# Kernel tuning notes

Hardware: AMD Instinct MI355X
Metric: run time of the kernel (lower is better)

The kernel has to match this reference:

```python
import jax, jax.numpy as jnp
import numpy as np

N_NODES = 50000
N_EDGES = 800000
IN_CH = 64
HID = 128
OUT_CH = 1
NUM_LAYERS = 3
NUM_TIMESTEPS = 3
EDGE_DIM = 25
NUM_GRAPHS = 1024
NEG = 0.01  # leaky_relu negative slope (torch default & GATConv arg)


def leaky(v):
    return jnp.where(v >= 0, v, NEG * v)


def seg_softmax(a, idx, n):
    # PyG softmax: exp(a - max_per_segment) / (sum_per_segment + 1e-16)
    m = jax.ops.segment_max(a, idx, num_segments=n)
    m = jnp.where(jnp.isfinite(m), m, 0.0)  # guard empty segments
    e = jnp.exp(a - m[idx])
    s = jax.ops.segment_sum(e, idx, num_segments=n)
    return e / (s[idx] + 1e-16)


def gru(inp, h, Wih, Whh, bih, bhh):
    gi = inp @ Wih.T + bih
    gh = h @ Whh.T + bhh
    ir, iz, inn = jnp.split(gi, 3, axis=-1)
    hr, hz, hn = jnp.split(gh, 3, axis=-1)
    r = jax.nn.sigmoid(ir + hr)
    z = jax.nn.sigmoid(iz + hz)
    n = jnp.tanh(inn + r * hn)
    return (1.0 - z) * n + z * h


def setup_inputs() -> dict:
    key = jax.random.key(0)
    ks = iter(jax.random.split(key, 40))

    def nrm(shape, s=0.05):
        return jax.random.normal(next(ks), shape, dtype=jnp.float32) * s

    L = NUM_LAYERS - 1
    H3 = 3 * HID
    inp = dict(
        x=jax.random.normal(next(ks), (N_NODES, IN_CH), dtype=jnp.float32),
        edge_index=jax.random.randint(next(ks), (2, N_EDGES), 0, N_NODES),
        batch=jnp.sort(jax.random.randint(next(ks), (N_NODES,), 0, NUM_GRAPHS)),
        W1=nrm((HID, IN_CH)), b1=jnp.zeros((HID,), jnp.float32),
        Wg1=nrm((HID, HID + EDGE_DIM)), att_l=nrm((HID,)), att_r=nrm((HID,)),
        Wg2=nrm((HID, HID)), bg=jnp.zeros((HID,), jnp.float32),
        Wih0=nrm((H3, HID)), Whh0=nrm((H3, HID)),
        bih0=jnp.zeros((H3,), jnp.float32), bhh0=jnp.zeros((H3,), jnp.float32),
        Wa=nrm((L, HID, HID)), att_src_a=nrm((L, HID)), att_dst_a=nrm((L, HID)),
        ba=jnp.zeros((L, HID), jnp.float32),
        Wih_a=nrm((L, H3, HID)), Whh_a=nrm((L, H3, HID)),
        bih_a=jnp.zeros((L, H3), jnp.float32), bhh_a=jnp.zeros((L, H3), jnp.float32),
        Wm=nrm((HID, HID)), att_src_m=nrm((HID,)), att_dst_m=nrm((HID,)),
        bm=jnp.zeros((HID,), jnp.float32),
        Wih_m=nrm((H3, HID)), Whh_m=nrm((H3, HID)),
        bih_m=jnp.zeros((H3,), jnp.float32), bhh_m=jnp.zeros((H3,), jnp.float32),
        W2=nrm((OUT_CH, HID)), b2=jnp.zeros((OUT_CH,), jnp.float32),
    )
    return inp


def reference(x, edge_index, batch, W1, b1, Wg1, att_l, att_r, Wg2, bg,
              Wih0, Whh0, bih0, bhh0, Wa, att_src_a, att_dst_a, ba,
              Wih_a, Whh_a, bih_a, bhh_a, Wm, att_src_m, att_dst_m, bm,
              Wih_m, Whh_m, bih_m, bhh_m, W2, b2):
    N = x.shape[0]
    E = edge_index.shape[1]
    src, dst = edge_index[0], edge_index[1]  # j -> i, aggregate at i=dst
    edge_attr = jnp.ones((E, EDGE_DIM), dtype=x.dtype)  # built inside original forward

    x = leaky(x @ W1.T + b1)

    # GATEConv: edge-feature-aware attention, sum aggregation
    xe = leaky(jnp.concatenate([x[src], edge_attr], axis=-1) @ Wg1.T)  # [E, H]
    a = seg_softmax(leaky(xe @ att_l + (x @ att_r)[dst]), dst, N)
    msg = (x[src] @ Wg2.T) * a[:, None]
    h = jax.nn.elu(jax.ops.segment_sum(msg, dst, num_segments=N) + bg)
    x = jax.nn.relu(gru(h, x, Wih0, Whh0, bih0, bhh0))

    # (num_layers - 1) GATConv + GRU atom updates
    for l in range(NUM_LAYERS - 1):
        xt = x @ Wa[l].T
        a = seg_softmax(leaky((xt @ att_src_a[l])[src] + (xt @ att_dst_a[l])[dst]), dst, N)
        h = jax.nn.elu(jax.ops.segment_sum(xt[src] * a[:, None], dst, num_segments=N) + ba[l])
        x = jax.nn.relu(gru(h, x, Wih_a[l], Whh_a[l], bih_a[l], bhh_a[l]))

    # attentive readout: bipartite GATConv node->molecule over num_timesteps
    out = jax.nn.relu(jax.ops.segment_sum(x, batch, num_segments=NUM_GRAPHS))
    xt = x @ Wm.T                 # shared lin for src (fixed across timesteps)
    a_src = xt @ att_src_m        # [N]
    for _ in range(NUM_TIMESTEPS):
        ot = out @ Wm.T           # shared lin for dst
        a = seg_softmax(leaky(a_src + (ot @ att_dst_m)[batch]), batch, NUM_GRAPHS)
        h = jax.nn.elu(jax.ops.segment_sum(xt * a[:, None], batch, num_segments=NUM_GRAPHS) + bm)
        out = jax.nn.relu(gru(h, out, Wih_m, Whh_m, bih_m, bhh_m))

    return out @ W2.T + b2
```

## Files before the change

kernel.cpp:

```cpp
#include <hip/hip_runtime.h>
#include <math.h>

#define NN 50000
#define NE 800000
#define NG 1024
#define HID 128

typedef __attribute__((ext_vector_type(8))) short short8;
typedef __attribute__((ext_vector_type(4))) unsigned short ushort4v;
typedef __attribute__((ext_vector_type(4))) float f32x4;

__device__ __forceinline__ float leakyf(float v){ return v >= 0.f ? v : 0.01f*v; }
__device__ __forceinline__ float sigmf(float v){ return 1.f/(1.f+expf(-v)); }
__device__ __forceinline__ float eluf(float v){ return v > 0.f ? v : expm1f(v); }
__device__ __forceinline__ unsigned short bf16rne(float f){
  union { float f; unsigned u; } v; v.f = f;
  return (unsigned short)((v.u + 0x7FFFu + ((v.u >> 16) & 1u)) >> 16);
}
__device__ __forceinline__ float bf2f(unsigned short h){
  union { unsigned u; float f; } v; v.u = ((unsigned)h) << 16; return v.f;
}
__device__ __forceinline__ short8 cvt8(const float* a){
  short8 r;
#pragma unroll
  for (int j=0;j<8;j++) r[j] = (short)bf16rne(a[j]);
  return r;
}

__global__ __launch_bounds__(256)
void pack_all(const float* W1, const float* Wg1, const float* Wg2, const float* Wa,
              const float* Wm, const float* Wih0, const float* Whh0,
              const float* Wih_a, const float* Whh_a, const float* Wih_m,
              const float* Whh_m, unsigned short* __restrict__ dst)
{
  int m = (int)blockIdx.y;
  int t = (int)blockIdx.x*4 + ((int)threadIdx.x>>6);
  int l = (int)threadIdx.x & 63;
  const float* src; int stride=128, M=128, K=128; size_t doff;
  switch(m){
    case 0:  src=W1;    stride=64;  K=64;  doff=0;      break;
    case 1:  src=Wg1;   stride=153;        doff=8192;   break;
    case 2:  src=Wg2;                      doff=24576;  break;
    case 3:  src=Wa;                       doff=40960;  break;
    case 4:  src=Wa+16384;                 doff=57344;  break;
    case 5:  src=Wm;                       doff=73728;  break;
    case 6:  src=Wih0;  M=384;             doff=90112;  break;
    case 7:  src=Whh0;  M=384;             doff=139264; break;
    case 8:  src=Wih_a; M=384;             doff=188416; break;
    case 9:  src=Whh_a; M=384;             doff=237568; break;
    case 10: src=Wih_a+49152; M=384;       doff=286720; break;
    case 11: src=Whh_a+49152; M=384;       doff=335872; break;
    case 12: src=Wih_m; M=384;             doff=385024; break;
    default: src=Whh_m; M=384;             doff=434176; break;
  }
  int tk = K/32;
  if (t >= (M/16)*tk) return;
  int ct = t / tk, kc = t % tk;
  int row = ct*16 + (l&15);
  int col = kc*32 + ((l>>4)<<3);
  unsigned short o[8];
#pragma unroll
  for (int j=0;j<8;j++) o[j] = bf16rne(src[(size_t)row*stride + col + j]);
  ushort4v* d = (ushort4v*)(dst + doff + (((size_t)t*64 + l)<<3));
  ushort4v d0; d0.x=o[0]; d0.y=o[1]; d0.z=o[2]; d0.w=o[3];
  ushort4v d1; d1.x=o[4]; d1.y=o[5]; d1.z=o[6]; d1.w=o[7];
  d[0]=d0; d[1]=d1;
}

__global__ __launch_bounds__(256)
void gemm_f32(const float* __restrict__ A, const unsigned short* __restrict__ Wp,
              const float* __restrict__ bias, float* __restrict__ Cf,
              unsigned short* __restrict__ Cb, int rows, int act)
{
  constexpr int K = 64, KC = 2;
  const int tid=(int)threadIdx.x, w=tid>>6, l=tid&63;
  const int fr=l&15, fq=l>>4;
  const int rt=w>>1, ch=w&1;
  const int bn = (int)blockIdx.x*32;
  const int ar = bn + rt*16 + fr;
  f32x4 acc[4];
#pragma unroll
  for (int j=0;j<4;j++) acc[j] = (f32x4){0.f,0.f,0.f,0.f};
#pragma unroll
  for (int kc=0;kc<KC;kc++){
    float a8[8];
    if (ar < rows){
      *(float4*)&a8[0] = *(const float4*)(A + (size_t)ar*K + kc*32 + fq*8);
      *(float4*)&a8[4] = *(const float4*)(A + (size_t)ar*K + kc*32 + fq*8 + 4);
    } else {
#pragma unroll
      for (int j=0;j<8;j++) a8[j]=0.f;
    }
    short8 fa = cvt8(a8);
#pragma unroll
    for (int j=0;j<4;j++){
      const short8 bfr = *(const short8*)(Wp + ((((size_t)(ch*4+j)*KC + kc)*64 + l)<<3));
      acc[j] = __builtin_amdgcn_mfma_f32_16x16x32_bf16(fa, bfr, acc[j], 0, 0, 0);
    }
  }
#pragma unroll
  for (int j=0;j<4;j++){
    int c = ch*64 + j*16 + fr;
    float bv = bias ? bias[c] : 0.f;
#pragma unroll
    for (int r4=0;r4<4;r4++){
      float o = acc[j][r4] + bv;
      if (act) o = leakyf(o);
      int r = bn + rt*16 + fq*4 + r4;
      if (r < rows){
        Cf[(size_t)r*HID + c] = o;
        Cb[(size_t)r*HID + c] = bf16rne(o);
      }
    }
  }
}

__global__ __launch_bounds__(256)
void gemm_b16(const unsigned short* __restrict__ Ab, const unsigned short* __restrict__ Wp,
              const float* __restrict__ bias, unsigned short* __restrict__ Cb,
              const float* __restrict__ v1, const float* __restrict__ v2,
              const float* __restrict__ va,
              float* __restrict__ s1, float* __restrict__ s2, int rows, int act)
{
  __shared__ float sd1[2][32];
  __shared__ float sd2[2][32];
  constexpr int KC = 4;
  const int tid=(int)threadIdx.x, w=tid>>6, l=tid&63;
  const int fr=l&15, fq=l>>4;
  const int rt=w>>1, ch=w&1;
  const int bn = (int)blockIdx.x*32;
  const int ar = bn + rt*16 + fr;
  f32x4 acc[4];
#pragma unroll
  for (int j=0;j<4;j++) acc[j] = (f32x4){0.f,0.f,0.f,0.f};
  float pa = 0.f;
#pragma unroll
  for (int kc=0;kc<KC;kc++){
    short8 fa;
    if (ar < rows) fa = *(const short8*)(Ab + (size_t)ar*HID + kc*32 + fq*8);
    else { short8 z = {0,0,0,0,0,0,0,0}; fa = z; }
    if (va && ch==0){
      float4 t0 = *(const float4*)(va + kc*32 + fq*8);
      float4 t1 = *(const float4*)(va + kc*32 + fq*8 + 4);
      pa += bf2f((unsigned short)fa[0])*t0.x + bf2f((unsigned short)fa[1])*t0.y
          + bf2f((unsigned short)fa[2])*t0.z + bf2f((unsigned short)fa[3])*t0.w
          + bf2f((unsigned short)fa[4])*t1.x + bf2f((unsigned short)fa[5])*t1.y
          + bf2f((unsigned short)fa[6])*t1.z + bf2f((unsigned short)fa[7])*t1.w;
    }
#pragma unroll
    for (int j=0;j<4;j++){
      const short8 bfr = *(const short8*)(Wp + ((((size_t)(ch*4+j)*KC + kc)*64 + l)<<3));
      acc[j] = __builtin_amdgcn_mfma_f32_16x16x32_bf16(fa, bfr, acc[j], 0, 0, 0);
    }
  }
  float dp1[4]={0.f,0.f,0.f,0.f}, dp2[4]={0.f,0.f,0.f,0.f};
#pragma unroll
  for (int j=0;j<4;j++){
    int c = ch*64 + j*16 + fr;
    float bv = bias ? bias[c] : 0.f;
    float w1 = v1 ? v1[c] : 0.f;
    float w2 = v2 ? v2[c] : 0.f;
#pragma unroll
    for (int r4=0;r4<4;r4++){
      float o = acc[j][r4] + bv;
      if (act) o = leakyf(o);
      dp1[r4] += o*w1; dp2[r4] += o*w2;
      int r = bn + rt*16 + fq*4 + r4;
      if (r < rows && Cb) Cb[(size_t)r*HID + c] = bf16rne(o);
    }
  }
  if (v1){
#pragma unroll
    for (int r4=0;r4<4;r4++){
#pragma unroll
      for (int m=1;m<16;m<<=1){ dp1[r4] += __shfl_xor(dp1[r4], m); dp2[r4] += __shfl_xor(dp2[r4], m); }
    }
    if (fr==0){
#pragma unroll
      for (int r4=0;r4<4;r4++){
        sd1[ch][rt*16 + fq*4 + r4] = dp1[r4];
        sd2[ch][rt*16 + fq*4 + r4] = dp2[r4];
      }
    }
    __syncthreads();
    if (tid < 32){
      int r = bn + tid;
      if (r < rows) s1[r] = sd1[0][tid] + sd1[1][tid];
    } else if (v2 && tid < 64){
      int r = bn + tid - 32;
      if (r < rows) s2[r] = sd2[0][tid-32] + sd2[1][tid-32];
    }
  }
  if (va && ch==0){
    pa += __shfl_xor(pa, 16); pa += __shfl_xor(pa, 32);
    if (fq==0){
      int r = bn + rt*16 + fr;
      if (r < rows) s2[r] = pa;
    }
  }
}

__global__ __launch_bounds__(512, 2)
void fused_gru(const unsigned short* __restrict__ Ahb, const unsigned short* __restrict__ Axb,
               const float* __restrict__ Axf,
               const unsigned short* __restrict__ Wi, const unsigned short* __restrict__ Wh,
               const float* __restrict__ bih, const float* __restrict__ bhh,
               float* __restrict__ outf, unsigned short* __restrict__ outb, int tiles)
{
  const int tid=(int)threadIdx.x, w=tid>>6, l=tid&63;
  const int fr=l&15, fq=l>>4;
  short8 wi_r[3][4], wh_r[3][4];
#pragma unroll
  for (int g=0;g<3;g++)
#pragma unroll
    for (int kc=0;kc<4;kc++){
      size_t o = ((((size_t)(g*8 + w)*4 + kc)*64 + l)<<3);
      wi_r[g][kc] = *(const short8*)(Wi + o);
      wh_r[g][kc] = *(const short8*)(Wh + o);
    }
  const int c0 = w*16 + fr;
  float bi0=bih[c0], bi1=bih[c0+128], bi2=bih[c0+256];
  float bh0=bhh[c0], bh1=bhh[c0+128], bh2=bhh[c0+256];

  int rt_end = min((int)blockIdx.x*8 + 8, tiles);
  for (int rt = (int)blockIdx.x*8; rt < rt_end; rt++){
    const int bn = rt*16;
    const int arow = bn + fr;
    f32x4 ai0={0,0,0,0}, ai1={0,0,0,0}, ai2={0,0,0,0};
    f32x4 ah0={0,0,0,0}, ah1={0,0,0,0}, ah2={0,0,0,0};
#pragma unroll
    for (int kc=0;kc<4;kc++){
      short8 fa = *(const short8*)(Ahb + (size_t)arow*HID + kc*32 + fq*8);
      short8 fx = *(const short8*)(Axb + (size_t)arow*HID + kc*32 + fq*8);
      ai0 = __builtin_amdgcn_mfma_f32_16x16x32_bf16(fa, wi_r[0][kc], ai0, 0, 0, 0);
      ai1 = __builtin_amdgcn_mfma_f32_16x16x32_bf16(fa, wi_r[1][kc], ai1, 0, 0, 0);
      ai2 = __builtin_amdgcn_mfma_f32_16x16x32_bf16(fa, wi_r[2][kc], ai2, 0, 0, 0);
      ah0 = __builtin_amdgcn_mfma_f32_16x16x32_bf16(fx, wh_r[0][kc], ah0, 0, 0, 0);
      ah1 = __builtin_amdgcn_mfma_f32_16x16x32_bf16(fx, wh_r[1][kc], ah1, 0, 0, 0);
      ah2 = __builtin_amdgcn_mfma_f32_16x16x32_bf16(fx, wh_r[2][kc], ah2, 0, 0, 0);
    }
#pragma unroll
    for (int r4=0;r4<4;r4++){
      int row = bn + fq*4 + r4;
      float rr = sigmf(ai0[r4] + bi0 + ah0[r4] + bh0);
      float zz = sigmf(ai1[r4] + bi1 + ah1[r4] + bh1);
      float nn = tanhf(ai2[r4] + bi2 + rr*(ah2[r4] + bh2));
      float hv = Axf[(size_t)row*HID + c0];
      float o = fmaxf((1.f - zz)*nn + zz*hv, 0.f);
      outf[(size_t)row*HID + c0] = o;
      outb[(size_t)row*HID + c0] = bf16rne(o);
    }
  }
}

__global__ __launch_bounds__(256)
void rowdot(const float* __restrict__ A, const float* __restrict__ v,
            const float* __restrict__ bias, float* __restrict__ out, int rows)
{
  int wave = (int)((blockIdx.x * blockDim.x + threadIdx.x) >> 6);
  int lane = (int)(threadIdx.x & 63);
  if (wave >= rows) return;
  float2 a  = ((const float2*)(A + (size_t)wave*HID))[lane];
  float2 vv = ((const float2*)v)[lane];
  float s = a.x*vv.x + a.y*vv.y;
  for (int off=32; off; off>>=1) s += __shfl_down(s, off);
  if (lane==0) out[wave] = s + (bias ? bias[0] : 0.f);
}

__global__ void colvec(const float* __restrict__ W, const float* __restrict__ v,
                       float* __restrict__ out)
{
  int k = (int)threadIdx.x;
  float s = 0.f;
  for (int j=0;j<HID;j++) s += W[j*HID+k]*v[j];
  out[k] = s;
}

__global__ void prep_cg(const float* __restrict__ Wg1, float* __restrict__ cg){
  int j = (int)threadIdx.x;
  float s = 0.f;
  for (int k=128;k<153;k++) s += Wg1[j*153+k];
  cg[j] = s;
}

__global__ void count_kernel(const int* __restrict__ idx, int* __restrict__ cnt, int n){
  int i = (int)(blockIdx.x*blockDim.x + threadIdx.x);
  if (i < n) atomicAdd(&cnt[idx[i]], 1);
}

__global__ __launch_bounds__(1024)
void scan_blocks(const int* __restrict__ cnt, int* __restrict__ off,
                 int* __restrict__ tot, int n)
{
  __shared__ int buf[1024];
  int i = (int)(blockIdx.x*1024 + threadIdx.x);
  int v = (i<n)? cnt[i] : 0;
  buf[threadIdx.x] = v;
  __syncthreads();
  for (int s=1;s<1024;s<<=1){
    int t = ((int)threadIdx.x >= s) ? buf[threadIdx.x - s] : 0;
    __syncthreads();
    buf[threadIdx.x] += t;
    __syncthreads();
  }
  if (i<n) off[i] = buf[threadIdx.x] - v;
  if (threadIdx.x==1023) tot[blockIdx.x] = buf[1023];
}

__global__ void scan_tot(int* __restrict__ tot, int* __restrict__ off_end, int nb){
  int lane = (int)threadIdx.x;
  int orig = (lane<nb)? tot[lane] : 0;
  int v = orig;
  for (int s=1;s<64;s<<=1){ int t = __shfl_up(v, s); if (lane>=s) v += t; }
  int total = __shfl(v, 63);
  if (lane<nb) tot[lane] = v - orig;
  if (lane==0) *off_end = total;
}

__global__ void scan_add(int* __restrict__ off, const int* __restrict__ tot, int n){
  int i = (int)(blockIdx.x*blockDim.x + threadIdx.x);
  if (i<n) off[i] += tot[i>>10];
}

__global__ void fill_kernel(const int* __restrict__ src, const int* __restrict__ dst,
                            const int* __restrict__ off, int* __restrict__ fill,
                            int* __restrict__ ssrc, int n){
  int e = (int)(blockIdx.x*blockDim.x + threadIdx.x);
  if (e < n){
    int d = dst[e];
    int p = off[d] + atomicAdd(&fill[d], 1);
    ssrc[p] = src[e];
  }
}

__global__ void graph_bounds(const int* __restrict__ batch, int* __restrict__ goff){
  int g = (int)(blockIdx.x*blockDim.x + threadIdx.x);
  if (g > NG) return;
  int lo=0, hi=NN;
  while (lo<hi){ int mid=(lo+hi)>>1; if (batch[mid] < g) lo=mid+1; else hi=mid; }
  goff[g] = lo;
}

__global__ __launch_bounds__(256)
void agg_edges(const int* __restrict__ off, const int* __restrict__ ssrc,
               const float* __restrict__ ls, const float* __restrict__ ld,
               const unsigned short* __restrict__ Mrows, const float* __restrict__ bias,
               unsigned short* __restrict__ outb, int n)
{
  __shared__ float wbuf[4][64];
  __shared__ int   sbuf[4][64];
  const int ws = (int)(threadIdx.x >> 6);
  int node = (int)((blockIdx.x * blockDim.x + threadIdx.x) >> 6);
  int lane = (int)(threadIdx.x & 63);
  if (node >= n) return;
  int e0 = off[node], e1 = off[node+1];
  float ldv = ld[node];
  const int h = lane >> 5, cl = lane & 31;
  float denom = 0.f;
  float4 acc = make_float4(0.f,0.f,0.f,0.f);
  for (int j0=e0; j0<e1; j0+=64){
    int cnt = min(64, e1-j0);
    float wv = 0.f; int sc = 0;
    if (lane < cnt){
      sc = ssrc[j0+lane];
      wv = expf(leakyf(ls[sc]+ldv));
    }
    denom += wv;
    wbuf[ws][lane] = wv;
    sbuf[ws][lane] = sc;
#pragma unroll 4
    for (int k2=0;k2<cnt;k2+=2){
      float wk = wbuf[ws][k2+h];
      int  sck = sbuf[ws][k2+h];
      uint2 mm = *(const uint2*)(Mrows + (size_t)sck*HID + cl*4);
      acc.x += wk*bf2f((unsigned short)(mm.x&0xffff));
      acc.y += wk*bf2f((unsigned short)(mm.x>>16));
      acc.z += wk*bf2f((unsigned short)(mm.y&0xffff));
      acc.w += wk*bf2f((unsigned short)(mm.y>>16));
    }
  }
  acc.x += __shfl_xor(acc.x, 32); acc.y += __shfl_xor(acc.y, 32);
  acc.z += __shfl_xor(acc.z, 32); acc.w += __shfl_xor(acc.w, 32);
  for (int o=32;o;o>>=1) denom += __shfl_xor(denom, o);
  if (h==0){
    float inv = 1.f/(denom + 1e-16f);
    float4 b = *(const float4*)(bias + cl*4);
    ushort4v ob;
    ob.x = bf16rne(eluf(acc.x*inv + b.x));
    ob.y = bf16rne(eluf(acc.y*inv + b.y));
    ob.z = bf16rne(eluf(acc.z*inv + b.z));
    ob.w = bf16rne(eluf(acc.w*inv + b.w));
    *(ushort4v*)(outb + (size_t)node*HID + cl*4) = ob;
  }
}

__global__ __launch_bounds__(256)
void graph_sum(const int* __restrict__ goff, const float* __restrict__ X,
               float* __restrict__ outf, unsigned short* __restrict__ outb)
{
  int g = (int)((blockIdx.x*blockDim.x + threadIdx.x) >> 6);
  int lane = (int)(threadIdx.x & 63);
  if (g >= NG) return;
  float2 acc = make_float2(0.f,0.f);
  for (int n=goff[g]; n<goff[g+1]; ++n){
    float2 v = ((const float2*)(X + (size_t)n*HID))[lane];
    acc.x += v.x; acc.y += v.y;
  }
  float ox = fmaxf(acc.x,0.f), oy = fmaxf(acc.y,0.f);
  ((float2*)(outf + (size_t)g*HID))[lane] = make_float2(ox, oy);
  unsigned u = (unsigned)bf16rne(ox) | ((unsigned)bf16rne(oy) << 16);
  *(unsigned*)(outb + (size_t)g*HID + lane*2) = u;
}

__global__ __launch_bounds__(256)
void graph_soft2(const int* __restrict__ goff, const float* __restrict__ asrc,
                 const float* __restrict__ gout, const float* __restrict__ vmd,
                 const unsigned short* __restrict__ Xt, const float* __restrict__ bias,
                 unsigned short* __restrict__ outb)
{
  __shared__ float wbuf[4][64];
  const int ws = (int)(threadIdx.x >> 6);
  int g = (int)((blockIdx.x*blockDim.x + threadIdx.x) >> 6);
  int lane = (int)(threadIdx.x & 63);
  if (g >= NG) return;
  float2 ov = ((const float2*)(gout + (size_t)g*HID))[lane];
  float2 vv = ((const float2*)vmd)[lane];
  float ad = ov.x*vv.x + ov.y*vv.y;
  for (int o=32;o;o>>=1) ad += __shfl_xor(ad, o);
  int n0 = goff[g], n1 = goff[g+1];
  const int h = lane >> 5, cl = lane & 31;
  float denom = 0.f;
  float4 acc = make_float4(0.f,0.f,0.f,0.f);
  for (int j0=n0; j0<n1; j0+=64){
    int cnt = min(64, n1-j0);
    float wv = 0.f;
    if (lane < cnt) wv = expf(leakyf(asrc[j0+lane]+ad));
    denom += wv;
    wbuf[ws][lane] = wv;
#pragma unroll 4
    for (int k2=0;k2<cnt;k2+=2){
      float wk = wbuf[ws][k2+h];
      int rowi = min(j0 + k2 + h, n1 - 1);
      uint2 mm = *(const uint2*)(Xt + (size_t)rowi*HID + cl*4);
      acc.x += wk*bf2f((unsigned short)(mm.x&0xffff));
      acc.y += wk*bf2f((unsigned short)(mm.x>>16));
      acc.z += wk*bf2f((unsigned short)(mm.y&0xffff));
      acc.w += wk*bf2f((unsigned short)(mm.y>>16));
    }
  }
  acc.x += __shfl_xor(acc.x, 32); acc.y += __shfl_xor(acc.y, 32);
  acc.z += __shfl_xor(acc.z, 32); acc.w += __shfl_xor(acc.w, 32);
  for (int o=32;o;o>>=1) denom += __shfl_xor(denom, o);
  if (h==0){
    float inv = 1.f/(denom + 1e-16f);
    float4 b = *(const float4*)(bias + cl*4);
    ushort4v ob;
    ob.x = bf16rne(eluf(acc.x*inv + b.x));
    ob.y = bf16rne(eluf(acc.y*inv + b.y));
    ob.z = bf16rne(eluf(acc.z*inv + b.z));
    ob.w = bf16rne(eluf(acc.w*inv + b.w));
    *(ushort4v*)(outb + (size_t)g*HID + cl*4) = ob;
  }
}

extern "C" void kernel_launch(void* const* d_in, const int* in_sizes, int n_in,
                              void* d_out, int out_size, void* d_ws, size_t ws_size,
                              hipStream_t stream)
{
  const float* x_in  = (const float*)d_in[0];
  const int*   ei    = (const int*)d_in[1];
  const int*   batch = (const int*)d_in[2];
  const float* W1    = (const float*)d_in[3];
  const float* b1    = (const float*)d_in[4];
  const float* Wg1   = (const float*)d_in[5];
  const float* att_l = (const float*)d_in[6];
  const float* att_r = (const float*)d_in[7];
  const float* Wg2   = (const float*)d_in[8];
  const float* bg    = (const float*)d_in[9];
  const float* Wih0  = (const float*)d_in[10];
  const float* Whh0  = (const float*)d_in[11];
  const float* bih0  = (const float*)d_in[12];
  const float* bhh0  = (const float*)d_in[13];
  const float* Wa    = (const float*)d_in[14];
  const float* att_src_a = (const float*)d_in[15];
  const float* att_dst_a = (const float*)d_in[16];
  const float* ba    = (const float*)d_in[17];
  const float* Wih_a = (const float*)d_in[18];
  const float* Whh_a = (const float*)d_in[19];
  const float* bih_a = (const float*)d_in[20];
  const float* bhh_a = (const float*)d_in[21];
  const float* Wm    = (const float*)d_in[22];
  const float* att_src_m = (const float*)d_in[23];
  const float* att_dst_m = (const float*)d_in[24];
  const float* bm    = (const float*)d_in[25];
  const float* Wih_m = (const float*)d_in[26];
  const float* Whh_m = (const float*)d_in[27];
  const float* bih_m = (const float*)d_in[28];
  const float* bhh_m = (const float*)d_in[29];
  const float* W2    = (const float*)d_in[30];
  const float* b2    = (const float*)d_in[31];
  (void)in_sizes; (void)n_in; (void)out_size; (void)ws_size;

  char* wsb = (char*)d_ws;
  size_t off = 0;
  auto alloc = [&](size_t bytes)->void* {
    void* p = wsb + off;
    off += (bytes + 255) & ~(size_t)255;
    return p;
  };
  float* f_x   = (float*)alloc((size_t)NN*HID*4);
  float* f_y   = (float*)alloc((size_t)NN*HID*4);
  unsigned short* f_xb = (unsigned short*)alloc((size_t)NN*HID*2);
  unsigned short* f_yb = (unsigned short*)alloc((size_t)NN*HID*2);
  unsigned short* f_h  = (unsigned short*)alloc((size_t)NN*HID*2);
  unsigned short* f_t  = (unsigned short*)alloc((size_t)NN*HID*2);
  float* f_s1  = (float*)alloc((size_t)NN*4);
  float* f_s2  = (float*)alloc((size_t)NN*4);
  float* g_of0 = (float*)alloc((size_t)NG*HID*4);
  float* g_of1 = (float*)alloc((size_t)NG*HID*4);
  unsigned short* g_ob0 = (unsigned short*)alloc((size_t)NG*HID*2);
  unsigned short* g_ob1 = (unsigned short*)alloc((size_t)NG*HID*2);
  unsigned short* g_hb  = (unsigned short*)alloc((size_t)NG*HID*2);
  float* w_cg  = (float*)alloc((size_t)HID*4);
  float* w_vmd = (float*)alloc((size_t)HID*4);
  unsigned short* w_pack = (unsigned short*)alloc((size_t)483328*2);
  int* i_cnt   = (int*)alloc((size_t)NN*4);
  int* i_off   = (int*)alloc((size_t)(NN+1)*4);
  int* i_fill  = (int*)alloc((size_t)NN*4);
  int* i_src   = (int*)alloc((size_t)NE*4);
  int* i_tot   = (int*)alloc((size_t)64*4);
  int* i_goff  = (int*)alloc((size_t)(NG+1)*4);

  const unsigned short* pk_W1   = w_pack + 0;
  const unsigned short* pk_g1   = w_pack + 8192;
  const unsigned short* pk_g2   = w_pack + 24576;
  const unsigned short* pk_wa0  = w_pack + 40960;
  const unsigned short* pk_wa1  = w_pack + 57344;
  const unsigned short* pk_wm   = w_pack + 73728;
  const unsigned short* pk_wih0 = w_pack + 90112;
  const unsigned short* pk_whh0 = w_pack + 139264;
  const unsigned short* pk_wiha0= w_pack + 188416;
  const unsigned short* pk_whha0= w_pack + 237568;
  const unsigned short* pk_wiha1= w_pack + 286720;
  const unsigned short* pk_whha1= w_pack + 335872;
  const unsigned short* pk_wihm = w_pack + 385024;
  const unsigned short* pk_whhm = w_pack + 434176;

  const int* e_src = ei;
  const int* e_dst = ei + NE;

  hipMemsetAsync(i_cnt, 0, (size_t)NN*4, stream);
  hipMemsetAsync(i_fill, 0, (size_t)NN*4, stream);

  const int NB = (NN + 1023)/1024;
  count_kernel<<<(NE+255)/256,256,0,stream>>>(e_dst, i_cnt, NE);
  scan_blocks<<<NB,1024,0,stream>>>(i_cnt, i_off, i_tot, NN);
  scan_tot<<<1,64,0,stream>>>(i_tot, i_off+NN, NB);
  scan_add<<<(NN+255)/256,256,0,stream>>>(i_off, i_tot, NN);
  fill_kernel<<<(NE+255)/256,256,0,stream>>>(e_src, e_dst, i_off, i_fill, i_src, NE);
  graph_bounds<<<(NG+1+255)/256,256,0,stream>>>(batch, i_goff);
  prep_cg<<<1,128,0,stream>>>(Wg1, w_cg);
  colvec<<<1,128,0,stream>>>(Wm, att_dst_m, w_vmd);
  pack_all<<<dim3(24,14),256,0,stream>>>(W1, Wg1, Wg2, Wa, Wm, Wih0, Whh0,
                                         Wih_a, Whh_a, Wih_m, Whh_m, w_pack);

  const int GB = (NN+31)/32;
  const int NT = NN/16;
  const int FB = (NT+7)/8;
  const int GT = NG/16;
  const int wavegrid_g = (NG*64)/256;

  gemm_f32<<<GB,256,0,stream>>>(x_in, pk_W1, b1, f_x, f_xb, NN, 1);

  float* curf = f_x;  unsigned short* curb = f_xb;
  float* nxtf = f_y;  unsigned short* nxtb = f_yb;

  gemm_b16<<<GB,256,0,stream>>>(curb, pk_g1, w_cg, nullptr,
                                att_l, nullptr, att_r, f_s1, f_s2, NN, 1);
  gemm_b16<<<GB,256,0,stream>>>(curb, pk_g2, nullptr, f_t,
                                nullptr,nullptr,nullptr,nullptr,nullptr, NN, 0);
  agg_edges<<<(NN+3)/4,256,0,stream>>>(i_off, i_src, f_s1, f_s2, f_t, bg, f_h, NN);
  fused_gru<<<FB,512,0,stream>>>(f_h, curb, curf, pk_wih0, pk_whh0, bih0, bhh0,
                                 nxtf, nxtb, NT);
  { float* t=curf; curf=nxtf; nxtf=t; unsigned short* tb=curb; curb=nxtb; nxtb=tb; }

  for (int l=0;l<2;l++){
    gemm_b16<<<GB,256,0,stream>>>(curb, l ? pk_wa1 : pk_wa0, nullptr, f_t,
                                  att_src_a + l*HID, att_dst_a + l*HID, nullptr,
                                  f_s1, f_s2, NN, 0);
    agg_edges<<<(NN+3)/4,256,0,stream>>>(i_off, i_src, f_s1, f_s2, f_t, ba + l*HID, f_h, NN);
    fused_gru<<<FB,512,0,stream>>>(f_h, curb, curf,
                                   l ? pk_wiha1 : pk_wiha0, l ? pk_whha1 : pk_whha0,
                                   bih_a + l*384, bhh_a + l*384, nxtf, nxtb, NT);
    { float* t=curf; curf=nxtf; nxtf=t; unsigned short* tb=curb; curb=nxtb; nxtb=tb; }
  }

  graph_sum<<<wavegrid_g,256,0,stream>>>(i_goff, curf, g_of0, g_ob0);
  gemm_b16<<<GB,256,0,stream>>>(curb, pk_wm, nullptr, f_t,
                                att_src_m, nullptr, nullptr, f_s1, nullptr, NN, 0);
  float* gcf = g_of0; unsigned short* gcb = g_ob0;
  float* gnf = g_of1; unsigned short* gnb = g_ob1;
  for (int t=0;t<3;t++){
    graph_soft2<<<wavegrid_g,256,0,stream>>>(i_goff, f_s1, gcf, w_vmd, f_t, bm, g_hb);
    fused_gru<<<(GT+7)/8,512,0,stream>>>(g_hb, gcb, gcf, pk_wihm, pk_whhm,
                                         bih_m, bhh_m, gnf, gnb, GT);
    { float* tf=gcf; gcf=gnf; gnf=tf; unsigned short* tb=gcb; gcb=gnb; gnb=tb; }
  }

  rowdot<<<wavegrid_g,256,0,stream>>>(gcf, W2, b2, (float*)d_out, NG);
}
```

Measured before the change: 664.5 us.

## Widen gather loads, prefetch GRU tiles, use fast math intrinsics, halve tiles per block

```diff
diff --git a/kernel.cpp b/kernel.cpp
--- a/kernel.cpp
+++ b/kernel.cpp
@@ -11,8 +11,10 @@
 typedef __attribute__((ext_vector_type(4))) float f32x4;
 
 __device__ __forceinline__ float leakyf(float v){ return v >= 0.f ? v : 0.01f*v; }
-__device__ __forceinline__ float sigmf(float v){ return 1.f/(1.f+expf(-v)); }
-__device__ __forceinline__ float eluf(float v){ return v > 0.f ? v : expm1f(v); }
+__device__ __forceinline__ float frcp(float x){ return __builtin_amdgcn_rcpf(x); }
+__device__ __forceinline__ float fsigm(float v){ return frcp(1.f + __expf(-v)); }
+__device__ __forceinline__ float ftanh(float v){ return 1.f - 2.f*frcp(1.f + __expf(2.f*v)); }
+__device__ __forceinline__ float eluf(float v){ return v > 0.f ? v : __expf(v) - 1.f; }
 __device__ __forceinline__ unsigned short bf16rne(float f){
   union { float f; unsigned u; } v; v.f = f;
   return (unsigned short)((v.u + 0x7FFFu + ((v.u >> 16) & 1u)) >> 16);
@@ -222,34 +224,55 @@
   float bi0=bih[c0], bi1=bih[c0+128], bi2=bih[c0+256];
   float bh0=bhh[c0], bh1=bhh[c0+128], bh2=bhh[c0+256];
 
-  int rt_end = min((int)blockIdx.x*8 + 8, tiles);
-  for (int rt = (int)blockIdx.x*8; rt < rt_end; rt++){
-    const int bn = rt*16;
-    const int arow = bn + fr;
+  int rt = (int)blockIdx.x*4;
+  int rt_end = min(rt + 4, tiles);
+  if (rt >= tiles) return;
+  short8 fa[4], fx[4];
+  {
+    const int arow = rt*16 + fr;
+#pragma unroll
+    for (int kc=0;kc<4;kc++){
+      fa[kc] = *(const short8*)(Ahb + (size_t)arow*HID + kc*32 + fq*8);
+      fx[kc] = *(const short8*)(Axb + (size_t)arow*HID + kc*32 + fq*8);
+    }
+  }
+  for (; rt < rt_end; rt++){
+    short8 nfa[4], nfx[4];
+    if (rt+1 < rt_end){
+      const int arow = (rt+1)*16 + fr;
+#pragma unroll
+      for (int kc=0;kc<4;kc++){
+        nfa[kc] = *(const short8*)(Ahb + (size_t)arow*HID + kc*32 + fq*8);
+        nfx[kc] = *(const short8*)(Axb + (size_t)arow*HID + kc*32 + fq*8);
+      }
+    }
+    float hv[4];
+#pragma unroll
+    for (int r4=0;r4<4;r4++) hv[r4] = Axf[(size_t)(rt*16 + fq*4 + r4)*HID + c0];
+
     f32x4 ai0={0,0,0,0}, ai1={0,0,0,0}, ai2={0,0,0,0};
     f32x4 ah0={0,0,0,0}, ah1={0,0,0,0}, ah2={0,0,0,0};
 #pragma unroll
     for (int kc=0;kc<4;kc++){
-      short8 fa = *(const short8*)(Ahb + (size_t)arow*HID + kc*32 + fq*8);
-      short8 fx = *(const short8*)(Axb + (size_t)arow*HID + kc*32 + fq*8);
-      ai0 = __builtin_amdgcn_mfma_f32_16x16x32_bf16(fa, wi_r[0][kc], ai0, 0, 0, 0);
-      ai1 = __builtin_amdgcn_mfma_f32_16x16x32_bf16(fa, wi_r[1][kc], ai1, 0, 0, 0);
-      ai2 = __builtin_amdgcn_mfma_f32_16x16x32_bf16(fa, wi_r[2][kc], ai2, 0, 0, 0);
-      ah0 = __builtin_amdgcn_mfma_f32_16x16x32_bf16(fx, wh_r[0][kc], ah0, 0, 0, 0);
-      ah1 = __builtin_amdgcn_mfma_f32_16x16x32_bf16(fx, wh_r[1][kc], ah1, 0, 0, 0);
-      ah2 = __builtin_amdgcn_mfma_f32_16x16x32_bf16(fx, wh_r[2][kc], ah2, 0, 0, 0);
+      ai0 = __builtin_amdgcn_mfma_f32_16x16x32_bf16(fa[kc], wi_r[0][kc], ai0, 0, 0, 0);
+      ai1 = __builtin_amdgcn_mfma_f32_16x16x32_bf16(fa[kc], wi_r[1][kc], ai1, 0, 0, 0);
+      ai2 = __builtin_amdgcn_mfma_f32_16x16x32_bf16(fa[kc], wi_r[2][kc], ai2, 0, 0, 0);
+      ah0 = __builtin_amdgcn_mfma_f32_16x16x32_bf16(fx[kc], wh_r[0][kc], ah0, 0, 0, 0);
+      ah1 = __builtin_amdgcn_mfma_f32_16x16x32_bf16(fx[kc], wh_r[1][kc], ah1, 0, 0, 0);
+      ah2 = __builtin_amdgcn_mfma_f32_16x16x32_bf16(fx[kc], wh_r[2][kc], ah2, 0, 0, 0);
     }
 #pragma unroll
     for (int r4=0;r4<4;r4++){
-      int row = bn + fq*4 + r4;
-      float rr = sigmf(ai0[r4] + bi0 + ah0[r4] + bh0);
-      float zz = sigmf(ai1[r4] + bi1 + ah1[r4] + bh1);
-      float nn = tanhf(ai2[r4] + bi2 + rr*(ah2[r4] + bh2));
-      float hv = Axf[(size_t)row*HID + c0];
-      float o = fmaxf((1.f - zz)*nn + zz*hv, 0.f);
+      int row = rt*16 + fq*4 + r4;
+      float rr = fsigm(ai0[r4] + bi0 + ah0[r4] + bh0);
+      float zz = fsigm(ai1[r4] + bi1 + ah1[r4] + bh1);
+      float nn = ftanh(ai2[r4] + bi2 + rr*(ah2[r4] + bh2));
+      float o = fmaxf((1.f - zz)*nn + zz*hv[r4], 0.f);
       outf[(size_t)row*HID + c0] = o;
       outb[(size_t)row*HID + c0] = bf16rne(o);
     }
+#pragma unroll
+    for (int kc=0;kc<4;kc++){ fa[kc]=nfa[kc]; fx[kc]=nfx[kc]; }
   }
 }
 
@@ -355,42 +378,51 @@
   if (node >= n) return;
   int e0 = off[node], e1 = off[node+1];
   float ldv = ld[node];
-  const int h = lane >> 5, cl = lane & 31;
+  const int g4 = lane >> 4, cl = lane & 15;
   float denom = 0.f;
-  float4 acc = make_float4(0.f,0.f,0.f,0.f);
+  float acc[8] = {0.f,0.f,0.f,0.f,0.f,0.f,0.f,0.f};
   for (int j0=e0; j0<e1; j0+=64){
     int cnt = min(64, e1-j0);
     float wv = 0.f; int sc = 0;
     if (lane < cnt){
       sc = ssrc[j0+lane];
-      wv = expf(leakyf(ls[sc]+ldv));
+      wv = __expf(leakyf(ls[sc]+ldv));
     }
     denom += wv;
     wbuf[ws][lane] = wv;
     sbuf[ws][lane] = sc;
-#pragma unroll 4
-    for (int k2=0;k2<cnt;k2+=2){
-      float wk = wbuf[ws][k2+h];
-      int  sck = sbuf[ws][k2+h];
-      uint2 mm = *(const uint2*)(Mrows + (size_t)sck*HID + cl*4);
-      acc.x += wk*bf2f((unsigned short)(mm.x&0xffff));
-      acc.y += wk*bf2f((unsigned short)(mm.x>>16));
-      acc.z += wk*bf2f((unsigned short)(mm.y&0xffff));
-      acc.w += wk*bf2f((unsigned short)(mm.y>>16));
-    }
-  }
-  acc.x += __shfl_xor(acc.x, 32); acc.y += __shfl_xor(acc.y, 32);
-  acc.z += __shfl_xor(acc.z, 32); acc.w += __shfl_xor(acc.w, 32);
+#pragma unroll 2
+    for (int k4=0;k4<cnt;k4+=4){
+      float wk = wbuf[ws][k4+g4];
+      int  sck = sbuf[ws][k4+g4];
+      uint4 mm = *(const uint4*)(Mrows + (size_t)sck*HID + cl*8);
+      acc[0] += wk*bf2f((unsigned short)(mm.x&0xffff));
+      acc[1] += wk*bf2f((unsigned short)(mm.x>>16));
+      acc[2] += wk*bf2f((unsigned short)(mm.y&0xffff));
+      acc[3] += wk*bf2f((unsigned short)(mm.y>>16));
+      acc[4] += wk*bf2f((unsigned short)(mm.z&0xffff));
+      acc[5] += wk*bf2f((unsigned short)(mm.z>>16));
+      acc[6] += wk*bf2f((unsigned short)(mm.w&0xffff));
+      acc[7] += wk*bf2f((unsigned short)(mm.w>>16));
+    }
+  }
+#pragma unroll
+  for (int j=0;j<8;j++){ acc[j] += __shfl_xor(acc[j], 16); acc[j] += __shfl_xor(acc[j], 32); }
   for (int o=32;o;o>>=1) denom += __shfl_xor(denom, o);
-  if (h==0){
-    float inv = 1.f/(denom + 1e-16f);
-    float4 b = *(const float4*)(bias + cl*4);
-    ushort4v ob;
-    ob.x = bf16rne(eluf(acc.x*inv + b.x));
-    ob.y = bf16rne(eluf(acc.y*inv + b.y));
-    ob.z = bf16rne(eluf(acc.z*inv + b.z));
-    ob.w = bf16rne(eluf(acc.w*inv + b.w));
-    *(ushort4v*)(outb + (size_t)node*HID + cl*4) = ob;
+  if (g4==0){
+    float inv = frcp(denom + 1e-16f);
+    float4 b0 = *(const float4*)(bias + cl*8);
+    float4 b1 = *(const float4*)(bias + cl*8 + 4);
+    float o0=eluf(acc[0]*inv+b0.x), o1=eluf(acc[1]*inv+b0.y);
+    float o2=eluf(acc[2]*inv+b0.z), o3=eluf(acc[3]*inv+b0.w);
+    float o4=eluf(acc[4]*inv+b1.x), o5=eluf(acc[5]*inv+b1.y);
+    float o6=eluf(acc[6]*inv+b1.z), o7=eluf(acc[7]*inv+b1.w);
+    uint4 u;
+    u.x = (unsigned)bf16rne(o0) | ((unsigned)bf16rne(o1)<<16);
+    u.y = (unsigned)bf16rne(o2) | ((unsigned)bf16rne(o3)<<16);
+    u.z = (unsigned)bf16rne(o4) | ((unsigned)bf16rne(o5)<<16);
+    u.w = (unsigned)bf16rne(o6) | ((unsigned)bf16rne(o7)<<16);
+    *(uint4*)(outb + (size_t)node*HID + cl*8) = u;
   }
 }
 
@@ -428,38 +460,47 @@
   float ad = ov.x*vv.x + ov.y*vv.y;
   for (int o=32;o;o>>=1) ad += __shfl_xor(ad, o);
   int n0 = goff[g], n1 = goff[g+1];
-  const int h = lane >> 5, cl = lane & 31;
+  const int g4 = lane >> 4, cl = lane & 15;
   float denom = 0.f;
-  float4 acc = make_float4(0.f,0.f,0.f,0.f);
+  float acc[8] = {0.f,0.f,0.f,0.f,0.f,0.f,0.f,0.f};
   for (int j0=n0; j0<n1; j0+=64){
     int cnt = min(64, n1-j0);
     float wv = 0.f;
-    if (lane < cnt) wv = expf(leakyf(asrc[j0+lane]+ad));
+    if (lane < cnt) wv = __expf(leakyf(asrc[j0+lane]+ad));
     denom += wv;
     wbuf[ws][lane] = wv;
-#pragma unroll 4
-    for (int k2=0;k2<cnt;k2+=2){
-      float wk = wbuf[ws][k2+h];
-      int rowi = min(j0 + k2 + h, n1 - 1);
-      uint2 mm = *(const uint2*)(Xt + (size_t)rowi*HID + cl*4);
-      acc.x += wk*bf2f((unsigned short)(mm.x&0xffff));
-      acc.y += wk*bf2f((unsigned short)(mm.x>>16));
-      acc.z += wk*bf2f((unsigned short)(mm.y&0xffff));
-      acc.w += wk*bf2f((unsigned short)(mm.y>>16));
-    }
-  }
-  acc.x += __shfl_xor(acc.x, 32); acc.y += __shfl_xor(acc.y, 32);
-  acc.z += __shfl_xor(acc.z, 32); acc.w += __shfl_xor(acc.w, 32);
+#pragma unroll 2
+    for (int k4=0;k4<cnt;k4+=4){
+      float wk = wbuf[ws][k4+g4];
+      int rowi = min(j0 + k4 + g4, n1 - 1);
+      uint4 mm = *(const uint4*)(Xt + (size_t)rowi*HID + cl*8);
+      acc[0] += wk*bf2f((unsigned short)(mm.x&0xffff));
+      acc[1] += wk*bf2f((unsigned short)(mm.x>>16));
+      acc[2] += wk*bf2f((unsigned short)(mm.y&0xffff));
+      acc[3] += wk*bf2f((unsigned short)(mm.y>>16));
+      acc[4] += wk*bf2f((unsigned short)(mm.z&0xffff));
+      acc[5] += wk*bf2f((unsigned short)(mm.z>>16));
+      acc[6] += wk*bf2f((unsigned short)(mm.w&0xffff));
+      acc[7] += wk*bf2f((unsigned short)(mm.w>>16));
+    }
+  }
+#pragma unroll
+  for (int j=0;j<8;j++){ acc[j] += __shfl_xor(acc[j], 16); acc[j] += __shfl_xor(acc[j], 32); }
   for (int o=32;o;o>>=1) denom += __shfl_xor(denom, o);
-  if (h==0){
-    float inv = 1.f/(denom + 1e-16f);
-    float4 b = *(const float4*)(bias + cl*4);
-    ushort4v ob;
-    ob.x = bf16rne(eluf(acc.x*inv + b.x));
-    ob.y = bf16rne(eluf(acc.y*inv + b.y));
-    ob.z = bf16rne(eluf(acc.z*inv + b.z));
-    ob.w = bf16rne(eluf(acc.w*inv + b.w));
-    *(ushort4v*)(outb + (size_t)g*HID + cl*4) = ob;
+  if (g4==0){
+    float inv = frcp(denom + 1e-16f);
+    float4 b0 = *(const float4*)(bias + cl*8);
+    float4 b1 = *(const float4*)(bias + cl*8 + 4);
+    float o0=eluf(acc[0]*inv+b0.x), o1=eluf(acc[1]*inv+b0.y);
+    float o2=eluf(acc[2]*inv+b0.z), o3=eluf(acc[3]*inv+b0.w);
+    float o4=eluf(acc[4]*inv+b1.x), o5=eluf(acc[5]*inv+b1.y);
+    float o6=eluf(acc[6]*inv+b1.z), o7=eluf(acc[7]*inv+b1.w);
+    uint4 u;
+    u.x = (unsigned)bf16rne(o0) | ((unsigned)bf16rne(o1)<<16);
+    u.y = (unsigned)bf16rne(o2) | ((unsigned)bf16rne(o3)<<16);
+    u.z = (unsigned)bf16rne(o4) | ((unsigned)bf16rne(o5)<<16);
+    u.w = (unsigned)bf16rne(o6) | ((unsigned)bf16rne(o7)<<16);
+    *(uint4*)(outb + (size_t)g*HID + cl*8) = u;
   }
 }
 
@@ -566,7 +607,7 @@
 
   const int GB = (NN+31)/32;
   const int NT = NN/16;
-  const int FB = (NT+7)/8;
+  const int FB = (NT+3)/4;
   const int GT = NG/16;
   const int wavegrid_g = (NG*64)/256;
 
@@ -602,7 +643,7 @@
   float* gnf = g_of1; unsigned short* gnb = g_ob1;
   for (int t=0;t<3;t++){
     graph_soft2<<<wavegrid_g,256,0,stream>>>(i_goff, f_s1, gcf, w_vmd, f_t, bm, g_hb);
-    fused_gru<<<(GT+7)/8,512,0,stream>>>(g_hb, gcb, gcf, pk_wihm, pk_whhm,
+    fused_gru<<<(GT+3)/4,512,0,stream>>>(g_hb, gcb, gcf, pk_wihm, pk_whhm,
                                          bih_m, bhh_m, gnf, gnb, GT);
     { float* tf=gcf; gcf=gnf; gnf=tf; unsigned short* tb=gcb; gcb=gnb; gnb=tb; }
   }
```

After: 614.0 us. 7.6% less time.
